# Kernel tuning notes

Measured on AMD Instinct MI355X. Metric: run time of the kernel, lower is better.

## Reference

```python
import jax, jax.numpy as jnp
import numpy as np

NUM_CLASSES = 1000
FEAT_DIM = 256
MOMENTUM = 0.999
WARMUP_STEPS = 200


def setup_inputs() -> dict:
    key = jax.random.key(0)
    k1, k2, k3, k4, k5 = jax.random.split(key, 5)
    N, B, K = 200000, 64, 100
    features = jax.random.normal(k1, (N, FEAT_DIM), jnp.float32)
    labels = jax.random.randint(k2, (N,), 0, NUM_CLASSES)
    labels_per_image = jax.random.randint(k3, (B, K), 0, NUM_CLASSES)
    prototypes = jax.random.normal(k4, (NUM_CLASSES, FEAT_DIM), jnp.float32)
    init_mask = jax.random.randint(k5, (NUM_CLASSES,), 0, 2).astype(jnp.int32)
    cooccurrence = jnp.zeros((NUM_CLASSES, NUM_CLASSES), jnp.float32)
    return dict(features=features, labels=labels, labels_per_image=labels_per_image,
                prototypes=prototypes, init_mask=init_mask, cooccurrence=cooccurrence,
                step=5000)


def reference(features, labels, labels_per_image, prototypes, init_mask, cooccurrence, step):
    C = prototypes.shape[0]
    progress = min(1.0, float(step) / max(1, WARMUP_STEPS * 10))
    m = 0.99 + (MOMENTUM - 0.99) * progress

    # F.normalize(features, dim=-1) with eps=1e-12
    fn = features / jnp.clip(jnp.linalg.norm(features, axis=-1, keepdims=True), 1e-12)

    # per-class scatter-mean (replaces Python loop over labels.unique())
    counts = jax.ops.segment_sum(jnp.ones(labels.shape, jnp.float32), labels, num_segments=C)  # [C]
    sums = jax.ops.segment_sum(fn, labels, num_segments=C)                                      # [C, D]
    mean = sums / jnp.maximum(counts, 1.0)[:, None]

    present = (counts > 0)[:, None]          # class appears in this batch
    inited = (init_mask > 0)[:, None]        # prototype already initialized
    ema = m * prototypes + (1.0 - m) * mean
    new_protos = jnp.where(present & inited, ema, jnp.where(present & ~inited, mean, prototypes))
    new_init = ((init_mask > 0) | (counts > 0)).astype(jnp.int32)

    # co-occurrence: presence matrix P[B,C]; pair (ci,cj) gets +1 each direction per image
    B, K = labels_per_image.shape
    rows = jnp.repeat(jnp.arange(B), K)
    P = jnp.zeros((B, C), jnp.float32).at[rows, labels_per_image.reshape(-1)].set(1.0)
    cooc_add = (P.T @ P) * (1.0 - jnp.eye(C, dtype=jnp.float32))
    new_cooc = cooccurrence + cooc_add

    return new_protos, new_init, new_cooc
```

## Files before the change

### kernel.cpp

```cpp
#include <hip/hip_runtime.h>
#include <hip/hip_fp16.h>

#define NC 1000
#define FD 256
#define KPI 100
#define CAP 512

union H4 { __half2 h[2]; uint2 u; };

__global__ __launch_bounds__(256) void k_norm_scatter(
    const float* __restrict__ feat, const int* __restrict__ labels, int n,
    const int* __restrict__ lpi, int bk,
    int* __restrict__ cursor, unsigned long long* __restrict__ M,
    uint2* __restrict__ buckets) {
    int tid = threadIdx.x;
    int lane = tid & 63;
    int w = tid >> 6;
    int gw = blockIdx.x * 4 + w;
    int gid = blockIdx.x * 256 + tid;
    int nw = gridDim.x * 4;

    if (gid < bk) atomicOr(&M[lpi[gid]], 1ull << (gid / KPI));

    const float4* f4 = (const float4*)feat;
    for (int r0 = gw * 2; r0 < n; r0 += nw * 2) {
        int r1 = r0 + 1;
        bool ok1 = r1 < n;
        float4 a = f4[(size_t)r0 * 64 + lane];
        float4 b = f4[(size_t)(ok1 ? r1 : r0) * 64 + lane];
        float s0 = a.x * a.x + a.y * a.y + a.z * a.z + a.w * a.w;
        float s1 = b.x * b.x + b.y * b.y + b.z * b.z + b.w * b.w;
        #pragma unroll
        for (int o = 32; o; o >>= 1) {
            s0 += __shfl_xor(s0, o);
            s1 += __shfl_xor(s1, o);
        }
        float sc0 = 1.0f / fmaxf(sqrtf(s0), 1e-12f);
        float sc1 = 1.0f / fmaxf(sqrtf(s1), 1e-12f);

        int lab0 = 0, lab1 = 0, pos0 = 0, pos1 = 0;
        if (lane == 0) {
            lab0 = labels[r0];
            pos0 = atomicAdd(&cursor[lab0], 1);
            if (ok1) {
                lab1 = labels[r1];
                pos1 = atomicAdd(&cursor[lab1], 1);
            }
        }
        lab0 = __shfl(lab0, 0); pos0 = __shfl(pos0, 0);
        lab1 = __shfl(lab1, 0); pos1 = __shfl(pos1, 0);

        H4 p0, p1;
        p0.h[0] = __floats2half2_rn(a.x * sc0, a.y * sc0);
        p0.h[1] = __floats2half2_rn(a.z * sc0, a.w * sc0);
        p1.h[0] = __floats2half2_rn(b.x * sc1, b.y * sc1);
        p1.h[1] = __floats2half2_rn(b.z * sc1, b.w * sc1);
        if (pos0 < CAP) buckets[((size_t)lab0 * CAP + pos0) * 64 + lane] = p0.u;
        if (ok1 && pos1 < CAP) buckets[((size_t)lab1 * CAP + pos1) * 64 + lane] = p1.u;
    }
}

__global__ __launch_bounds__(1024, 8) void k_finalize(
    const uint2* __restrict__ buckets, const int* __restrict__ cursor,
    const float* __restrict__ protos, const int* __restrict__ init_mask,
    const int* __restrict__ step,
    const unsigned long long* __restrict__ M,
    const float* __restrict__ cooc_in,
    float* __restrict__ out_protos, float* __restrict__ out_init,
    float* __restrict__ out_cooc) {
    int c = blockIdx.x;
    int tid = threadIdx.x;
    int lane = tid & 63;
    int w = tid >> 6;
    int cnt = cursor[c];
    int cntd = cnt > CAP ? CAP : cnt;

    const uint2* base = buckets + (size_t)c * CAP * 64;
    float ax = 0.f, ay = 0.f, az = 0.f, aw = 0.f;

    for (int r = w; r < cntd; r += 32) {
        int r2 = r + 16;
        bool ok2 = r2 < cntd;
        uint2 q0 = base[(size_t)r * 64 + lane];
        uint2 q1 = base[(size_t)(ok2 ? r2 : r) * 64 + lane];
        H4 h0, h1; h0.u = q0; h1.u = q1;
        float2 f00 = __half22float2(h0.h[0]);
        float2 f01 = __half22float2(h0.h[1]);
        ax += f00.x; ay += f00.y; az += f01.x; aw += f01.y;
        if (ok2) {
            float2 f10 = __half22float2(h1.h[0]);
            float2 f11 = __half22float2(h1.h[1]);
            ax += f10.x; ay += f10.y; az += f11.x; aw += f11.y;
        }
    }

    __shared__ float4 sh4[1024];
    sh4[w * 64 + lane] = make_float4(ax, ay, az, aw);
    __syncthreads();

    if (tid < 64) {
        float4 s = make_float4(0.f, 0.f, 0.f, 0.f);
        #pragma unroll
        for (int q = 0; q < 16; q++) {
            float4 t = sh4[q * 64 + tid];
            s.x += t.x; s.y += t.y; s.z += t.z; s.w += t.w;
        }
        float inv = 1.0f / fmaxf((float)cnt, 1.0f);
        bool present = cnt > 0;
        bool inited = init_mask[c] > 0;
        float prog = fminf(1.0f, (float)step[0] / 2000.0f);
        float m = 0.99f + (0.999f - 0.99f) * prog;

        const float4* p4 = (const float4*)(protos + (size_t)c * FD);
        float4 p = p4[tid];
        float4 o;
        #define EMA1(mc, pc) (present ? (inited ? (m * (pc) + (1.0f - m) * ((mc) * inv)) \
                                                : ((mc) * inv)) : (pc))
        o.x = EMA1(s.x, p.x); o.y = EMA1(s.y, p.y);
        o.z = EMA1(s.z, p.z); o.w = EMA1(s.w, p.w);
        #undef EMA1
        ((float4*)(out_protos + (size_t)c * FD))[tid] = o;
        if (tid == 0) out_init[c] = (inited || present) ? 1.0f : 0.0f;
    }

    if (tid < NC) {
        unsigned long long mi = M[c];
        float add = (c == tid) ? 0.0f : (float)__popcll(mi & M[tid]);
        out_cooc[c * NC + tid] = cooc_in[c * NC + tid] + add;
    }
}

extern "C" void kernel_launch(void* const* d_in, const int* in_sizes, int n_in,
                              void* d_out, int out_size, void* d_ws, size_t ws_size,
                              hipStream_t stream) {
    const float* feat      = (const float*)d_in[0];
    const int*   labels    = (const int*)d_in[1];
    const int*   lpi       = (const int*)d_in[2];
    const float* protos    = (const float*)d_in[3];
    const int*   init_mask = (const int*)d_in[4];
    const float* cooc      = (const float*)d_in[5];
    const int*   step      = (const int*)d_in[6];

    int n  = in_sizes[1];
    int bk = in_sizes[2];

    float* out_protos = (float*)d_out;
    float* out_init   = out_protos + (size_t)NC * FD;
    float* out_cooc   = out_init + NC;

    char* ws = (char*)d_ws;
    int* cursor           = (int*)(ws);
    unsigned long long* M = (unsigned long long*)(ws + 4096);
    uint2* buckets        = (uint2*)(ws + 16384);

    hipMemsetAsync(d_ws, 0, 12288, stream);

    k_norm_scatter<<<2048, 256, 0, stream>>>(feat, labels, n, lpi, bk,
                                             cursor, M, buckets);
    k_finalize<<<NC, 1024, 0, stream>>>(buckets, cursor, protos, init_mask, step,
                                        M, cooc, out_protos, out_init, out_cooc);
}
```

Measured before the change: 341.6 us.

## Scatter row indices instead of fp16 features, gather and normalize per class

The first kernel now only bins row indices by label (plus the co-occurrence bitmask). Previously it normalized every feature row and wrote fp16 copies into per-class buckets. The per-class kernel gathers the original fp32 rows through the index list, normalizes them in-register and accumulates. This removes the intermediate bucket write and re-read, cutting global traffic and avoiding fp16 rounding. The cost is random row gathers and a smaller 512-thread block per class.

```diff
diff --git a/kernel.cpp b/kernel.cpp
--- a/kernel.cpp
+++ b/kernel.cpp
@@ -1,67 +1,27 @@
 #include <hip/hip_runtime.h>
-#include <hip/hip_fp16.h>
 
 #define NC 1000
 #define FD 256
 #define KPI 100
 #define CAP 512
 
-union H4 { __half2 h[2]; uint2 u; };
-
-__global__ __launch_bounds__(256) void k_norm_scatter(
-    const float* __restrict__ feat, const int* __restrict__ labels, int n,
+__global__ __launch_bounds__(256) void k_index(
+    const int* __restrict__ labels, int n,
     const int* __restrict__ lpi, int bk,
     int* __restrict__ cursor, unsigned long long* __restrict__ M,
-    uint2* __restrict__ buckets) {
-    int tid = threadIdx.x;
-    int lane = tid & 63;
-    int w = tid >> 6;
-    int gw = blockIdx.x * 4 + w;
-    int gid = blockIdx.x * 256 + tid;
-    int nw = gridDim.x * 4;
-
+    int* __restrict__ idxbuf) {
+    int gid = blockIdx.x * 256 + threadIdx.x;
     if (gid < bk) atomicOr(&M[lpi[gid]], 1ull << (gid / KPI));
-
-    const float4* f4 = (const float4*)feat;
-    for (int r0 = gw * 2; r0 < n; r0 += nw * 2) {
-        int r1 = r0 + 1;
-        bool ok1 = r1 < n;
-        float4 a = f4[(size_t)r0 * 64 + lane];
-        float4 b = f4[(size_t)(ok1 ? r1 : r0) * 64 + lane];
-        float s0 = a.x * a.x + a.y * a.y + a.z * a.z + a.w * a.w;
-        float s1 = b.x * b.x + b.y * b.y + b.z * b.z + b.w * b.w;
-        #pragma unroll
-        for (int o = 32; o; o >>= 1) {
-            s0 += __shfl_xor(s0, o);
-            s1 += __shfl_xor(s1, o);
-        }
-        float sc0 = 1.0f / fmaxf(sqrtf(s0), 1e-12f);
-        float sc1 = 1.0f / fmaxf(sqrtf(s1), 1e-12f);
-
-        int lab0 = 0, lab1 = 0, pos0 = 0, pos1 = 0;
-        if (lane == 0) {
-            lab0 = labels[r0];
-            pos0 = atomicAdd(&cursor[lab0], 1);
-            if (ok1) {
-                lab1 = labels[r1];
-                pos1 = atomicAdd(&cursor[lab1], 1);
-            }
-        }
-        lab0 = __shfl(lab0, 0); pos0 = __shfl(pos0, 0);
-        lab1 = __shfl(lab1, 0); pos1 = __shfl(pos1, 0);
-
-        H4 p0, p1;
-        p0.h[0] = __floats2half2_rn(a.x * sc0, a.y * sc0);
-        p0.h[1] = __floats2half2_rn(a.z * sc0, a.w * sc0);
-        p1.h[0] = __floats2half2_rn(b.x * sc1, b.y * sc1);
-        p1.h[1] = __floats2half2_rn(b.z * sc1, b.w * sc1);
-        if (pos0 < CAP) buckets[((size_t)lab0 * CAP + pos0) * 64 + lane] = p0.u;
-        if (ok1 && pos1 < CAP) buckets[((size_t)lab1 * CAP + pos1) * 64 + lane] = p1.u;
+    if (gid < n) {
+        int lab = labels[gid];
+        int pos = atomicAdd(&cursor[lab], 1);
+        if (pos < CAP) idxbuf[lab * CAP + pos] = gid;
     }
 }
 
-__global__ __launch_bounds__(1024, 8) void k_finalize(
-    const uint2* __restrict__ buckets, const int* __restrict__ cursor,
+__global__ __launch_bounds__(512) void k_class(
+    const float* __restrict__ feat, int n, const int* __restrict__ idxbuf,
+    const int* __restrict__ cursor,
     const float* __restrict__ protos, const int* __restrict__ init_mask,
     const int* __restrict__ step,
     const unsigned long long* __restrict__ M,
@@ -73,35 +33,51 @@
     int lane = tid & 63;
     int w = tid >> 6;
     int cnt = cursor[c];
+    if (cnt < 0) cnt = 0;
     int cntd = cnt > CAP ? CAP : cnt;
 
-    const uint2* base = buckets + (size_t)c * CAP * 64;
-    float ax = 0.f, ay = 0.f, az = 0.f, aw = 0.f;
+    __shared__ int sidx[CAP];
+    for (int i = tid; i < cntd; i += 512) {
+        int v = idxbuf[c * CAP + i];
+        sidx[i] = (v < 0) ? 0 : (v >= n ? n - 1 : v);
+    }
+    __syncthreads();
 
-    for (int r = w; r < cntd; r += 32) {
-        int r2 = r + 16;
+    const float4* f4 = (const float4*)feat;
+    float4 acc = make_float4(0.f, 0.f, 0.f, 0.f);
+
+    for (int r = w; r < cntd; r += 16) {
+        int r2 = r + 8;
         bool ok2 = r2 < cntd;
-        uint2 q0 = base[(size_t)r * 64 + lane];
-        uint2 q1 = base[(size_t)(ok2 ? r2 : r) * 64 + lane];
-        H4 h0, h1; h0.u = q0; h1.u = q1;
-        float2 f00 = __half22float2(h0.h[0]);
-        float2 f01 = __half22float2(h0.h[1]);
-        ax += f00.x; ay += f00.y; az += f01.x; aw += f01.y;
+        int i0 = sidx[r];
+        int i1 = sidx[ok2 ? r2 : r];
+        float4 a = f4[(size_t)i0 * 64 + lane];
+        float4 b = f4[(size_t)i1 * 64 + lane];
+        float s0 = a.x * a.x + a.y * a.y + a.z * a.z + a.w * a.w;
+        float s1 = b.x * b.x + b.y * b.y + b.z * b.z + b.w * b.w;
+        #pragma unroll
+        for (int o = 32; o; o >>= 1) {
+            s0 += __shfl_xor(s0, o);
+            s1 += __shfl_xor(s1, o);
+        }
+        float sc0 = 1.0f / fmaxf(sqrtf(s0), 1e-12f);
+        float sc1 = 1.0f / fmaxf(sqrtf(s1), 1e-12f);
+        acc.x += a.x * sc0; acc.y += a.y * sc0;
+        acc.z += a.z * sc0; acc.w += a.w * sc0;
         if (ok2) {
-            float2 f10 = __half22float2(h1.h[0]);
-            float2 f11 = __half22float2(h1.h[1]);
-            ax += f10.x; ay += f10.y; az += f11.x; aw += f11.y;
+            acc.x += b.x * sc1; acc.y += b.y * sc1;
+            acc.z += b.z * sc1; acc.w += b.w * sc1;
         }
     }
 
-    __shared__ float4 sh4[1024];
-    sh4[w * 64 + lane] = make_float4(ax, ay, az, aw);
+    __shared__ float4 sh4[512];
+    sh4[w * 64 + lane] = acc;
     __syncthreads();
 
     if (tid < 64) {
         float4 s = make_float4(0.f, 0.f, 0.f, 0.f);
         #pragma unroll
-        for (int q = 0; q < 16; q++) {
+        for (int q = 0; q < 8; q++) {
             float4 t = sh4[q * 64 + tid];
             s.x += t.x; s.y += t.y; s.z += t.z; s.w += t.w;
         }
@@ -123,10 +99,10 @@
         if (tid == 0) out_init[c] = (inited || present) ? 1.0f : 0.0f;
     }
 
-    if (tid < NC) {
-        unsigned long long mi = M[c];
-        float add = (c == tid) ? 0.0f : (float)__popcll(mi & M[tid]);
-        out_cooc[c * NC + tid] = cooc_in[c * NC + tid] + add;
+    unsigned long long mi = M[c];
+    for (int j = tid; j < NC; j += 512) {
+        float add = (c == j) ? 0.0f : (float)__popcll(mi & M[j]);
+        out_cooc[c * NC + j] = cooc_in[c * NC + j] + add;
     }
 }
 
@@ -151,12 +127,12 @@
     char* ws = (char*)d_ws;
     int* cursor           = (int*)(ws);
     unsigned long long* M = (unsigned long long*)(ws + 4096);
-    uint2* buckets        = (uint2*)(ws + 16384);
+    int* idxbuf           = (int*)(ws + 16384);
 
     hipMemsetAsync(d_ws, 0, 12288, stream);
 
-    k_norm_scatter<<<2048, 256, 0, stream>>>(feat, labels, n, lpi, bk,
-                                             cursor, M, buckets);
-    k_finalize<<<NC, 1024, 0, stream>>>(buckets, cursor, protos, init_mask, step,
-                                        M, cooc, out_protos, out_init, out_cooc);
+    int blocks = (n + 255) / 256;
+    k_index<<<blocks, 256, 0, stream>>>(labels, n, lpi, bk, cursor, M, idxbuf);
+    k_class<<<NC, 512, 0, stream>>>(feat, n, idxbuf, cursor, protos, init_mask, step,
+                                    M, cooc, out_protos, out_init, out_cooc);
 }
```

After: 341.9 us. About the same (+0.1%).
